# Kernel tuning notes

Hardware: AMD Instinct MI355X
Metric: run time of the kernel (lower is better)

## Reference

```python
import jax, jax.numpy as jnp
import numpy as np

B, T, D = 8192, 32, 12        # batch, MAX_EVENTS, EVENT_DIM
Z, HE, HD = 128, 512, 1024    # z_dim, hidden_enc, hidden_dec


def _lstm(xs, h0, c0, W_ih, W_hh, b):
    """PyTorch-convention LSTM. xs: (T,B,in). Returns hs: (T,B,H)."""
    x_proj = jnp.einsum('tbi,gi->tbg', xs, W_ih) + b  # hoist input GEMM out of scan

    def step(carry, xp):
        h, c = carry
        gates = xp + h @ W_hh.T
        i, f, g, o = jnp.split(gates, 4, axis=-1)
        c = jax.nn.sigmoid(f) * c + jax.nn.sigmoid(i) * jnp.tanh(g)
        h = jax.nn.sigmoid(o) * jnp.tanh(c)
        return (h, c), h

    _, hs = jax.lax.scan(step, (h0, c0), x_proj)
    return hs


def setup_inputs() -> dict:
    key = jax.random.key(0)
    ks = jax.random.split(key, 20)
    g = lambda k, shape, s=0.05: (jax.random.normal(k, shape, dtype=jnp.float32) * s)
    return {
        'x': jax.random.normal(ks[0], (B, T, D), dtype=jnp.float32),
        'lengths': jax.random.randint(ks[1], (B,), 0, 33, dtype=jnp.int32),
        'eps': jax.random.normal(ks[2], (B, Z), dtype=jnp.float32),
        # encoder LSTM (bias = b_ih + b_hh fused)
        'W_ih_e': g(ks[3], (4 * HE, D)), 'W_hh_e': g(ks[4], (4 * HE, HE)), 'b_e': g(ks[5], (4 * HE,)),
        'W_mu': g(ks[6], (Z, HE)), 'b_mu': g(ks[7], (Z,)),
        'W_lv': g(ks[8], (Z, HE)), 'b_lv': g(ks[9], (Z,)),
        # decoder
        'W_h0': g(ks[10], (HD, Z)), 'b_h0': g(ks[11], (HD,)),
        'W_c0': g(ks[12], (HD, Z)), 'b_c0': g(ks[13], (HD,)),
        'start_token': jnp.zeros((D,), dtype=jnp.float32),
        'W_ih_d': g(ks[14], (4 * HD, D)), 'W_hh_d': g(ks[15], (4 * HD, HD)), 'b_d': g(ks[16], (4 * HD,)),
        'W_out': g(ks[17], (D, HD)), 'b_out': g(ks[18], (D,)),
    }


def reference(x, lengths, eps, W_ih_e, W_hh_e, b_e, W_mu, b_mu, W_lv, b_lv,
              W_h0, b_h0, W_c0, b_c0, start_token, W_ih_d, W_hh_d, b_d, W_out, b_out):
    Bx = x.shape[0]
    # ---- encoder: packed LSTM == take hidden state at step (len-1) ----
    xs = jnp.transpose(x, (1, 0, 2))  # (T,B,D)
    zeros_e = jnp.zeros((Bx, HE), dtype=x.dtype)
    hs_e = _lstm(xs, zeros_e, zeros_e, W_ih_e, W_hh_e, b_e)  # (T,B,HE)
    last = jnp.clip(lengths, 1, T) - 1                        # clamp(min=1)
    h_n = hs_e[last, jnp.arange(Bx)]                          # (B,HE)
    mu = h_n @ W_mu.T + b_mu
    logvar = h_n @ W_lv.T + b_lv
    z = mu + eps * jnp.exp(0.5 * logvar)
    # ---- decoder: teacher forcing (tf_ratio=1.0) ----
    h0 = jnp.tanh(z @ W_h0.T + b_h0)
    c0 = jnp.tanh(z @ W_c0.T + b_c0)
    start = jnp.broadcast_to(start_token, (1, Bx, D))
    x_in = jnp.concatenate([start, xs[:-1]], axis=0)          # (T,B,D) shifted right
    hs_d = _lstm(x_in, h0, c0, W_ih_d, W_hh_d, b_d)           # (T,B,HD)
    x_recon = jnp.transpose(hs_d @ W_out.T + b_out, (1, 0, 2))  # (B,T,D)
    return x_recon, mu, logvar, z
```

## Files before the change

kernel.cpp:

```cpp
#include <hip/hip_runtime.h>
#include <hip/hip_bf16.h>

#define BB 8192
#define TT 32
#define DD 12
#define ZZ 128
#define HE 512
#define HD 1024
#define KEp 640
#define KDp 1152

typedef unsigned short u16;
typedef __attribute__((ext_vector_type(8))) short bf16x8;
typedef __attribute__((ext_vector_type(4))) float f32x4;

__device__ __forceinline__ u16 f2bf(float f) {
    __hip_bfloat16 h = __float2bfloat16(f);
    return *reinterpret_cast<u16*>(&h);
}
__device__ __forceinline__ float bf2f(u16 u) {
    __hip_bfloat16 h;
    *reinterpret_cast<u16*>(&h) = u;
    return __bfloat162float(h);
}
__device__ __forceinline__ float sigmf(float x) { return 1.f / (1.f + __expf(-x)); }
__device__ __forceinline__ float tanh_(float x) {
    float ax = fabsf(x);
    float e = __expf(-2.f * ax);
    float t = (1.f - e) / (1.f + e);
    return copysignf(t, x);
}

__device__ __forceinline__ void gload_lds16(const void* g, void* l) {
    __builtin_amdgcn_global_load_lds(
        (const __attribute__((address_space(1))) void*)g,
        (__attribute__((address_space(3))) void*)l,
        16, 0, 0);
}

#define BAR() asm volatile("s_barrier" ::: "memory")
#define VMCNT(n) asm volatile("s_waitcnt vmcnt(" #n ")" ::: "memory")

#define REGION(dd, mat, kh) (((dd)*4 + (mat)*2 + (kh)) * 8192)

#define STAGE(dd, mat, kh, ktile) do { \
    const u16* Gp_ = (mat) ? W : A; \
    const int rb_ = (mat) ? bn : bm; \
    const int kc_ = (ktile)*64 + (kh)*32 + (tid & 3)*8; \
    u16* dst_ = &lds[REGION(dd, mat, kh) + tid*8]; \
    const u16* s0_ = Gp_ + (size_t)(rb_ + (tid >> 2)) * Kp + kc_; \
    gload_lds16(s0_, dst_); \
    gload_lds16(s0_ + (size_t)128 * Kp, dst_ + 4096); \
} while (0)

#define LDA4(mh, dd, kh) do { \
    const u16* bp_ = &lds[REGION(dd, 0, kh)]; \
    _Pragma("unroll") \
    for (int i_ = 0; i_ < 4; ++i_) \
        af[i_] = *(const bf16x8*)&bp_[(wm*128 + (mh)*64 + i_*16 + (lane & 15))*32 + (lane >> 4)*8]; \
} while (0)

#define LDB4(dd, kh) do { \
    const u16* bp_ = &lds[REGION(dd, 1, kh)]; \
    _Pragma("unroll") \
    for (int j_ = 0; j_ < 4; ++j_) \
        bf[j_] = *(const bf16x8*)&bp_[(wn*64 + j_*16 + (lane & 15))*32 + (lane >> 4)*8]; \
} while (0)

#define MFMA16(mh) do { \
    __builtin_amdgcn_s_setprio(1); \
    _Pragma("unroll") \
    for (int i_ = 0; i_ < 4; ++i_) \
    _Pragma("unroll") \
    for (int j_ = 0; j_ < 4; ++j_) \
        acc[(mh)*4 + i_][j_] = __builtin_amdgcn_mfma_f32_16x16x32_bf16( \
            af[i_], bf[j_], acc[(mh)*4 + i_][j_], 0, 0, 0); \
    __builtin_amdgcn_s_setprio(0); \
} while (0)

template<int MODE>
__global__ __launch_bounds__(512, 2)
void gemm256(const u16* __restrict__ A, const u16* __restrict__ W,
             int Kp, int NT, int H,
             float* __restrict__ Cst, u16* __restrict__ Aout,
             const float* __restrict__ bias, const int* __restrict__ lens,
             u16* __restrict__ HN, const float* __restrict__ X, int t)
{
    extern __shared__ u16 lds[];
    const int tid  = threadIdx.x;
    const int lane = tid & 63;
    const int wid  = tid >> 6;
    const int wm = wid >> 2, wn = wid & 3;
    const int bm = blockIdx.x * 256;
    const int bn = blockIdx.y * 256;

    f32x4 acc[8][4] = {};
    bf16x8 af[4], bf[4];

    STAGE(0, 0, 0, 0); STAGE(0, 1, 0, 0);
    STAGE(0, 0, 1, 0); STAGE(0, 1, 1, 0);
    STAGE(1, 0, 0, 1); STAGE(1, 1, 0, 1);
    VMCNT(4);
    BAR();

    const int NI = NT >> 1;
    for (int n = 0; n < NI; ++n) {
        const int t1 = 2*n + 1, t2 = 2*n + 2, t3 = 2*n + 3;
        const bool more = (t2 < NT);
        LDA4(0, 0, 0); LDB4(0, 0);
        STAGE(1, 0, 1, t1);
        BAR(); MFMA16(0); BAR();
        LDA4(1, 0, 0);
        STAGE(1, 1, 1, t1);
        BAR(); MFMA16(1); BAR();
        LDA4(0, 0, 1); LDB4(0, 1);
        if (more) STAGE(0, 0, 0, t2);
        BAR(); MFMA16(0); BAR();
        LDA4(1, 0, 1);
        if (more) STAGE(0, 1, 0, t2);
        BAR(); MFMA16(1);
        if (n == NI - 1) { VMCNT(0); } else { VMCNT(4); }
        BAR();
        LDA4(0, 1, 0); LDB4(1, 0);
        if (more) STAGE(0, 0, 1, t2);
        BAR(); MFMA16(0); BAR();
        LDA4(1, 1, 0);
        if (more) STAGE(0, 1, 1, t2);
        BAR(); MFMA16(1); BAR();
        LDA4(0, 1, 1); LDB4(1, 1);
        if (more) STAGE(1, 0, 0, t3);
        BAR(); MFMA16(0); BAR();
        LDA4(1, 1, 1);
        if (more) STAGE(1, 1, 0, t3);
        BAR(); MFMA16(1);
        if (n < NI - 1) { VMCNT(4); }
        BAR();
    }

    const int hcol = ((bn >> 6) + wn) * 16 + (lane & 15);
    const float bI = bias[hcol];
    const float bF = bias[H + hcol];
    const float bG = bias[2 * H + hcol];
    const float bO = bias[3 * H + hcol];
#pragma unroll
    for (int i = 0; i < 8; ++i) {
        const int rbase = bm + wm * 128 + i * 16 + (lane >> 4) * 4;
#pragma unroll
        for (int q = 0; q < 4; ++q) {
            const int r = rbase + q;
            float iv = sigmf(acc[i][0][q] + bI);
            float fv = sigmf(acc[i][1][q] + bF);
            float gv = tanh_(acc[i][2][q] + bG);
            float ov = sigmf(acc[i][3][q] + bO);
            float cn = fv * Cst[(size_t)r * H + hcol] + iv * gv;
            float h  = ov * tanh_(cn);
            Cst[(size_t)r * H + hcol] = cn;
            Aout[(size_t)r * Kp + hcol] = f2bf(h);
            if (MODE == 1) {
                int L = lens[r]; L = (L < 1) ? 1 : (L > TT ? TT : L);
                if (t == L - 1) HN[(size_t)r * H + hcol] = f2bf(h);
            }
        }
    }
    const int tx = (MODE == 1) ? t + 1 : t;
    if (bn == 0 && tx < TT) {
        for (int ii = tid; ii < 256 * DD; ii += 512) {
            const int rr = ii / DD, d = ii - rr * DD;
            const int r = bm + rr;
            Aout[(size_t)r * Kp + H + d] = f2bf(X[((size_t)r * TT + tx) * DD + d]);
        }
    }
}

__global__ __launch_bounds__(256, 2)
void gemm_bt(const u16* __restrict__ A, const u16* __restrict__ W,
             float* __restrict__ C, int N, int K)
{
    __shared__ u16 As[128 * 64];
    __shared__ u16 Ws[128 * 64];
    const int tid  = threadIdx.x;
    const int lane = tid & 63;
    const int wave = tid >> 6;
    const int wm = wave >> 1, wn = wave & 1;
    const int bm = blockIdx.x * 128;
    const int bn = blockIdx.y * 128;

    f32x4 acc[4][4] = {};
    const int lrow = lane >> 3;
    const int lcol = (lane & 7) * 8;

    for (int kt = 0; kt < K; kt += 64) {
#pragma unroll
        for (int c2 = 0; c2 < 4; ++c2) {
            const int chunk = wave * 4 + c2;
            const int row = chunk * 8 + lrow;
            gload_lds16(A + (size_t)(bm + row) * K + kt + lcol, &As[chunk * 512]);
            gload_lds16(W + (size_t)(bn + row) * K + kt + lcol, &Ws[chunk * 512]);
        }
        __syncthreads();
#pragma unroll
        for (int ks = 0; ks < 2; ++ks) {
            bf16x8 af[4], wf[4];
            const int ko = ks * 32 + (lane >> 4) * 8;
            const int rA = wm * 64 + (lane & 15);
            const int rW = wn * 64 + (lane & 15);
#pragma unroll
            for (int i = 0; i < 4; ++i)
                af[i] = *(const bf16x8*)&As[(rA + i * 16) * 64 + ko];
#pragma unroll
            for (int i = 0; i < 4; ++i)
                wf[i] = *(const bf16x8*)&Ws[(rW + i * 16) * 64 + ko];
#pragma unroll
            for (int i = 0; i < 4; ++i)
#pragma unroll
                for (int j = 0; j < 4; ++j)
                    acc[i][j] = __builtin_amdgcn_mfma_f32_16x16x32_bf16(
                        af[i], wf[j], acc[i][j], 0, 0, 0);
        }
        __syncthreads();
    }
    const int r0 = bm + wm * 64 + (lane >> 4) * 4;
    const int c0 = bn + wn * 64 + (lane & 15);
#pragma unroll
    for (int i = 0; i < 4; ++i)
#pragma unroll
        for (int j = 0; j < 4; ++j) {
            float* Cp = C + (size_t)(r0 + i * 16) * N + c0 + j * 16;
#pragma unroll
            for (int q = 0; q < 4; ++q)
                Cp[(size_t)q * N] = acc[i][j][q];
        }
}

__global__ void prep_wg(const float* __restrict__ Whh, const float* __restrict__ Wih,
                        u16* __restrict__ dst, int H, int Kc, int total)
{
    int idx = blockIdx.x * 256 + threadIdx.x;
    if (idx >= total) return;
    int np = idx / Kc, k = idx - np * Kc;
    int jblk = np >> 6, rem = np & 63;
    int gate = rem >> 4, jl = rem & 15;
    int j = jblk * 16 + jl;
    int srow = gate * H + j;
    float v = 0.f;
    if (k < H) v = Whh[(size_t)srow * H + k];
    else if (k < H + DD) v = Wih[srow * DD + (k - H)];
    dst[idx] = f2bf(v);
}

__global__ void prep_cat(const float* __restrict__ W0, const float* __restrict__ W1,
                         u16* __restrict__ dst, int rows0, int K, int total)
{
    int idx = blockIdx.x * 256 + threadIdx.x;
    if (idx >= total) return;
    int n = idx / K, k = idx - n * K;
    float v = (n < rows0) ? W0[(size_t)n * K + k] : W1[(size_t)(n - rows0) * K + k];
    dst[idx] = f2bf(v);
}

__global__ void prep_bf(const float* __restrict__ src, u16* __restrict__ dst, int total)
{
    int idx = blockIdx.x * 256 + threadIdx.x;
    if (idx < total) dst[idx] = f2bf(src[idx]);
}

__global__ void init_enc(u16* __restrict__ A, float* __restrict__ c, const float* __restrict__ x)
{
    int idx = blockIdx.x * 256 + threadIdx.x;
    int b = idx / KEp, j = idx - b * KEp;
    u16 v = 0;
    if (j >= HE && j < HE + DD) v = f2bf(x[(size_t)b * (TT * DD) + (j - HE)]);
    A[idx] = v;
    if (j < HE) c[(size_t)b * HE + j] = 0.f;
}

__global__ void zero_pads(u16* __restrict__ A, int ldK, int lo, int n, int total)
{
    int idx = blockIdx.x * 256 + threadIdx.x;
    if (idx >= total) return;
    int b = idx / n, j = idx - b * n;
    A[(size_t)b * ldK + lo + j] = 0;
}

__global__ void z_comp(const float* __restrict__ MV, const float* __restrict__ bmu,
                       const float* __restrict__ blv, const float* __restrict__ eps,
                       float* __restrict__ out, u16* __restrict__ Zbf)
{
    int idx = blockIdx.x * 256 + threadIdx.x;
    int b = idx >> 7, zc = idx & (ZZ - 1);
    float mu = MV[(size_t)b * 256 + zc] + bmu[zc];
    float lv = MV[(size_t)b * 256 + ZZ + zc] + blv[zc];
    float z = mu + eps[idx] * __expf(0.5f * lv);
    const size_t XR = (size_t)BB * TT * DD;
    out[XR + idx] = mu;
    out[XR + (size_t)BB * ZZ + idx] = lv;
    out[XR + 2 * (size_t)BB * ZZ + idx] = z;
    Zbf[idx] = f2bf(z);
}

__global__ void hc_init(const float* __restrict__ HC, const float* __restrict__ bh0,
                        const float* __restrict__ bc0, u16* __restrict__ A,
                        float* __restrict__ c)
{
    int idx = blockIdx.x * 256 + threadIdx.x;
    int b = idx >> 10, j = idx & (HD - 1);
    float h0 = tanh_(HC[(size_t)b * 2048 + j] + bh0[j]);
    float c0 = tanh_(HC[(size_t)b * 2048 + HD + j] + bc0[j]);
    A[(size_t)b * KDp + j] = f2bf(h0);
    c[idx] = c0;
}

__global__ void init_dec(u16* __restrict__ A, const float* __restrict__ st)
{
    int idx = blockIdx.x * 256 + threadIdx.x;
    int b = idx >> 7, j = idx & 127;
    A[(size_t)b * KDp + HD + j] = (j < DD) ? f2bf(st[j]) : (u16)0;
}

__global__ void outproj2(const u16* __restrict__ A, const u16* __restrict__ Wb,
                         const float* __restrict__ bout, float* __restrict__ xr, int t)
{
    int gid = blockIdx.x * 256 + threadIdx.x;
    int b = gid >> 6;
    int lane = threadIdx.x & 63;
    const u16* h = A + (size_t)b * KDp;
    const int k0 = lane * 16;
    bf16x8 h0 = *(const bf16x8*)&h[k0];
    bf16x8 h1 = *(const bf16x8*)&h[k0 + 8];
    float hv[16];
#pragma unroll
    for (int k = 0; k < 8; ++k) { hv[k] = bf2f((u16)h0[k]); hv[k + 8] = bf2f((u16)h1[k]); }
    float acc[DD];
#pragma unroll
    for (int d = 0; d < DD; ++d) {
        const u16* w = Wb + d * HD + k0;
        bf16x8 w0 = *(const bf16x8*)&w[0];
        bf16x8 w1 = *(const bf16x8*)&w[8];
        float a = 0.f;
#pragma unroll
        for (int k = 0; k < 8; ++k)
            a += hv[k] * bf2f((u16)w0[k]) + hv[k + 8] * bf2f((u16)w1[k]);
        acc[d] = a;
    }
#pragma unroll
    for (int off = 32; off > 0; off >>= 1)
#pragma unroll
        for (int d = 0; d < DD; ++d)
            acc[d] += __shfl_xor(acc[d], off);
    if (lane < DD)
        xr[((size_t)b * TT + t) * DD + lane] = acc[lane] + bout[lane];
}

extern "C" void kernel_launch(void* const* d_in, const int* in_sizes, int n_in,
                              void* d_out, int out_size, void* d_ws, size_t ws_size,
                              hipStream_t stream)
{
    const float* x    = (const float*)d_in[0];
    const int*   lens = (const int*)d_in[1];
    const float* eps  = (const float*)d_in[2];
    const float* Wihe = (const float*)d_in[3];
    const float* Whhe = (const float*)d_in[4];
    const float* be   = (const float*)d_in[5];
    const float* Wmu  = (const float*)d_in[6];
    const float* bmu  = (const float*)d_in[7];
    const float* Wlv  = (const float*)d_in[8];
    const float* blv  = (const float*)d_in[9];
    const float* Wh0  = (const float*)d_in[10];
    const float* bh0  = (const float*)d_in[11];
    const float* Wc0  = (const float*)d_in[12];
    const float* bc0  = (const float*)d_in[13];
    const float* st   = (const float*)d_in[14];
    const float* Wihd = (const float*)d_in[15];
    const float* Whhd = (const float*)d_in[16];
    const float* bd   = (const float*)d_in[17];
    const float* Wout = (const float*)d_in[18];
    const float* bout = (const float*)d_in[19];
    float* out = (float*)d_out;

    char* ws = (char*)d_ws;
    size_t o = 0;
    u16*   WCE = (u16*)(ws + o); o += (size_t)2048 * KEp * 2;
    u16*   WCD = (u16*)(ws + o); o += (size_t)4096 * KDp * 2;
    u16*   WMV = (u16*)(ws + o); o += (size_t)256 * 512 * 2;
    u16*   WHC = (u16*)(ws + o); o += (size_t)2048 * 128 * 2;
    u16*   WOB = (u16*)(ws + o); o += 32768;
    u16*   AE0 = (u16*)(ws + o); o += (size_t)BB * KEp * 2;
    u16*   AE1 = (u16*)(ws + o); o += (size_t)BB * KEp * 2;
    u16*   AD0 = (u16*)(ws + o); o += (size_t)BB * KDp * 2;
    u16*   AD1 = (u16*)(ws + o); o += (size_t)BB * KDp * 2;
    float* CE  = (float*)(ws + o); o += (size_t)BB * HE * 4;
    float* CD  = (float*)(ws + o); o += (size_t)BB * HD * 4;
    u16*   HNb = (u16*)(ws + o); o += (size_t)BB * HE * 2;
    float* MV  = (float*)(ws + o); o += (size_t)BB * 256 * 4;
    u16*   Zbf = (u16*)(ws + o); o += (size_t)BB * ZZ * 2;
    float* HC  = (float*)(ws + o); o += (size_t)BB * 2048 * 4;

    hipFuncSetAttribute((const void*)gemm256<1>,
                        hipFuncAttributeMaxDynamicSharedMemorySize, 131072);
    hipFuncSetAttribute((const void*)gemm256<2>,
                        hipFuncAttributeMaxDynamicSharedMemorySize, 131072);

    prep_wg<<<(2048 * KEp + 255) / 256, 256, 0, stream>>>(Whhe, Wihe, WCE, HE, KEp, 2048 * KEp);
    prep_wg<<<(4096 * KDp + 255) / 256, 256, 0, stream>>>(Whhd, Wihd, WCD, HD, KDp, 4096 * KDp);
    prep_cat<<<(256 * 512 + 255) / 256, 256, 0, stream>>>(Wmu, Wlv, WMV, ZZ, HE, 256 * 512);
    prep_cat<<<(2048 * 128 + 255) / 256, 256, 0, stream>>>(Wh0, Wc0, WHC, HD, ZZ, 2048 * 128);
    prep_bf<<<(12 * HD + 255) / 256, 256, 0, stream>>>(Wout, WOB, 12 * HD);
    init_enc<<<(BB * KEp) / 256, 256, 0, stream>>>(AE0, CE, x);
    zero_pads<<<(BB * 116 + 255) / 256, 256, 0, stream>>>(AE1, KEp, HE + DD, 116, BB * 116);
    zero_pads<<<(BB * 116 + 255) / 256, 256, 0, stream>>>(AD1, KDp, HD + DD, 116, BB * 116);

    u16* AE[2] = {AE0, AE1};
    for (int t = 0; t < TT; ++t) {
        gemm256<1><<<dim3(BB / 256, 2048 / 256), 512, 131072, stream>>>(
            AE[t & 1], WCE, KEp, 10, HE, CE, AE[1 - (t & 1)], be, lens, HNb, x, t);
    }

    gemm_bt<<<dim3(BB / 128, 256 / 128), 256, 0, stream>>>(HNb, WMV, MV, 256, 512);
    z_comp<<<(BB * ZZ) / 256, 256, 0, stream>>>(MV, bmu, blv, eps, out, Zbf);
    gemm_bt<<<dim3(BB / 128, 2048 / 128), 256, 0, stream>>>(Zbf, WHC, HC, 2048, 128);
    hc_init<<<(BB * HD) / 256, 256, 0, stream>>>(HC, bh0, bc0, AD0, CD);
    init_dec<<<(BB * 128) / 256, 256, 0, stream>>>(AD0, st);

    u16* AD[2] = {AD0, AD1};
    for (int t = 0; t < TT; ++t) {
        gemm256<2><<<dim3(BB / 256, 4096 / 256), 512, 131072, stream>>>(
            AD[t & 1], WCD, KDp, 18, HD, CD, AD[1 - (t & 1)], bd, nullptr, nullptr, x, t);
        outproj2<<<(BB * 64) / 256, 256, 0, stream>>>(AD[1 - (t & 1)], WOB, bout, out, t);
    }
}
```

Measured before the change: 5.054 ms.

## Use XOR-swizzled 64-wide LDS tiles with simpler double-buffered staging

The LDS layout changes from separate 32-column half-tiles per k-half to full 64-column rows per k-tile, with an XOR swizzle on the 16-byte chunk index to avoid bank conflicts in the fragment reads. Staging is simplified to whole-tile double buffering: the next tile is issued at the start of each half-iteration and waited on with vmcnt(0) at the end. This removes the finer-grained prefetch interleaving, so there is less overlap of global loads with MFMA work and a risk of exposed memory latency, traded against fewer LDS bank conflicts.

```diff
diff --git a/kernel.cpp b/kernel.cpp
--- a/kernel.cpp
+++ b/kernel.cpp
@@ -41,30 +41,35 @@
 #define BAR() asm volatile("s_barrier" ::: "memory")
 #define VMCNT(n) asm volatile("s_waitcnt vmcnt(" #n ")" ::: "memory")
 
-#define REGION(dd, mat, kh) (((dd)*4 + (mat)*2 + (kh)) * 8192)
-
-#define STAGE(dd, mat, kh, ktile) do { \
+#define REGION(dd, mat) (((dd)*2 + (mat)) * 16384)
+
+#define STAGE(dd, mat, ktile) do { \
     const u16* Gp_ = (mat) ? W : A; \
     const int rb_ = (mat) ? bn : bm; \
-    const int kc_ = (ktile)*64 + (kh)*32 + (tid & 3)*8; \
-    u16* dst_ = &lds[REGION(dd, mat, kh) + tid*8]; \
-    const u16* s0_ = Gp_ + (size_t)(rb_ + (tid >> 2)) * Kp + kc_; \
-    gload_lds16(s0_, dst_); \
-    gload_lds16(s0_ + (size_t)128 * Kp, dst_ + 4096); \
+    const int r0_ = tid >> 3; \
+    const int ks_ = (ktile)*64 + (((tid & 7) ^ (r0_ & 7)) << 3); \
+    u16* dst_ = &lds[REGION(dd, mat) + tid*8]; \
+    const u16* s0_ = Gp_ + (size_t)(rb_ + r0_) * Kp + ks_; \
+    gload_lds16(s0_,                    dst_); \
+    gload_lds16(s0_ + (size_t)64  * Kp, dst_ + 4096); \
+    gload_lds16(s0_ + (size_t)128 * Kp, dst_ + 8192); \
+    gload_lds16(s0_ + (size_t)192 * Kp, dst_ + 12288); \
 } while (0)
 
 #define LDA4(mh, dd, kh) do { \
-    const u16* bp_ = &lds[REGION(dd, 0, kh)]; \
+    const u16* bp_ = &lds[REGION(dd, 0)]; \
+    const int sw_ = ((((kh)*4 + (lane >> 4)) ^ (lane & 7)) << 3); \
     _Pragma("unroll") \
     for (int i_ = 0; i_ < 4; ++i_) \
-        af[i_] = *(const bf16x8*)&bp_[(wm*128 + (mh)*64 + i_*16 + (lane & 15))*32 + (lane >> 4)*8]; \
+        af[i_] = *(const bf16x8*)&bp_[(wm*128 + (mh)*64 + i_*16 + (lane & 15))*64 + sw_]; \
 } while (0)
 
 #define LDB4(dd, kh) do { \
-    const u16* bp_ = &lds[REGION(dd, 1, kh)]; \
+    const u16* bp_ = &lds[REGION(dd, 1)]; \
+    const int sw_ = ((((kh)*4 + (lane >> 4)) ^ (lane & 7)) << 3); \
     _Pragma("unroll") \
     for (int j_ = 0; j_ < 4; ++j_) \
-        bf[j_] = *(const bf16x8*)&bp_[(wn*64 + j_*16 + (lane & 15))*32 + (lane >> 4)*8]; \
+        bf[j_] = *(const bf16x8*)&bp_[(wn*64 + j_*16 + (lane & 15))*64 + sw_]; \
 } while (0)
 
 #define MFMA16(mh) do { \
@@ -97,44 +102,32 @@
     f32x4 acc[8][4] = {};
     bf16x8 af[4], bf[4];
 
-    STAGE(0, 0, 0, 0); STAGE(0, 1, 0, 0);
-    STAGE(0, 0, 1, 0); STAGE(0, 1, 1, 0);
-    STAGE(1, 0, 0, 1); STAGE(1, 1, 0, 1);
-    VMCNT(4);
+    STAGE(0, 0, 0); STAGE(0, 1, 0);
+    VMCNT(0);
     BAR();
 
     const int NI = NT >> 1;
     for (int n = 0; n < NI; ++n) {
-        const int t1 = 2*n + 1, t2 = 2*n + 2, t3 = 2*n + 3;
+        const int t1 = 2*n + 1, t2 = 2*n + 2;
         const bool more = (t2 < NT);
         LDA4(0, 0, 0); LDB4(0, 0);
-        STAGE(1, 0, 1, t1);
+        STAGE(1, 0, t1); STAGE(1, 1, t1);
         BAR(); MFMA16(0); BAR();
         LDA4(1, 0, 0);
-        STAGE(1, 1, 1, t1);
         BAR(); MFMA16(1); BAR();
         LDA4(0, 0, 1); LDB4(0, 1);
-        if (more) STAGE(0, 0, 0, t2);
         BAR(); MFMA16(0); BAR();
         LDA4(1, 0, 1);
-        if (more) STAGE(0, 1, 0, t2);
-        BAR(); MFMA16(1);
-        if (n == NI - 1) { VMCNT(0); } else { VMCNT(4); }
-        BAR();
+        BAR(); MFMA16(1); VMCNT(0); BAR();
         LDA4(0, 1, 0); LDB4(1, 0);
-        if (more) STAGE(0, 0, 1, t2);
+        if (more) { STAGE(0, 0, t2); STAGE(0, 1, t2); }
         BAR(); MFMA16(0); BAR();
         LDA4(1, 1, 0);
-        if (more) STAGE(0, 1, 1, t2);
         BAR(); MFMA16(1); BAR();
         LDA4(0, 1, 1); LDB4(1, 1);
-        if (more) STAGE(1, 0, 0, t3);
         BAR(); MFMA16(0); BAR();
         LDA4(1, 1, 1);
-        if (more) STAGE(1, 1, 0, t3);
-        BAR(); MFMA16(1);
-        if (n < NI - 1) { VMCNT(4); }
-        BAR();
+        BAR(); MFMA16(1); VMCNT(0); BAR();
     }
 
     const int hcol = ((bn >> 6) + wn) * 16 + (lane & 15);
```

New measurement: 4.859 ms. 3.9% less time.
